# Kernel optimization log

Measured on AMD Instinct MI355X. Metric: run time of the kernel, lower is better.

The kernel has to match this reference:

```python
import jax, jax.numpy as jnp
import numpy as np


def _gauss_kernel(k, sigma):
    t = jnp.arange(k, dtype=jnp.float32) - (k - 1) / 2.0
    w = jnp.exp(-0.5 * (t / sigma) ** 2)
    return w / jnp.sum(w)


def setup_inputs() -> dict:
    key = jax.random.key(0)
    x = jax.random.normal(key, (8, 1, 16, 512, 512), dtype=jnp.float32)
    return {"x": x}


def _forward(x):
    b, c, n, h, w = x.shape
    imgs = x.reshape(b * n * c, 1, h, w)  # fuse batch/frame loop into one batched conv
    # Sobel-style vertical/horizontal 3x3 kernels (cross-correlation, as in torch F.conv2d)
    sobel = jnp.stack([
        jnp.array([[0., -1., 0.], [0., 0., 0.], [0., 1., 0.]], jnp.float32),
        jnp.array([[0., 0., 0.], [-1., 0., 1.], [0., 0., 0.]], jnp.float32),
    ])[:, None]  # (2,1,3,3)
    dn = jax.lax.conv_dimension_numbers(imgs.shape, sobel.shape, ('NCHW', 'OIHW', 'NCHW'))
    g = jax.lax.conv_general_dilated(imgs, sobel, (1, 1), [(1, 1), (1, 1)], dimension_numbers=dn)
    grad = jnp.sqrt(g[:, 0:1] ** 2 + g[:, 1:2] ** 2 + 1e-6)  # (b*n,1,h,w)
    # torchvision GaussianBlur(kernel_size=(7,13), sigma=(9,11)): ksize 7 along width,
    # 13 along height; sigma sampled U(9,11) at call time -> fixed to 10.0 for determinism.
    kx = _gauss_kernel(7, 10.0)
    ky = _gauss_kernel(13, 10.0)
    p = jnp.pad(grad, ((0, 0), (0, 0), (6, 6), (3, 3)), mode='reflect')  # torchvision reflect pad
    dnb = jax.lax.conv_dimension_numbers(p.shape, (1, 1, 1, 7), ('NCHW', 'OIHW', 'NCHW'))
    blur = jax.lax.conv_general_dilated(p, kx.reshape(1, 1, 1, 7), (1, 1), [(0, 0), (0, 0)], dimension_numbers=dnb)
    blur = jax.lax.conv_general_dilated(blur, ky.reshape(1, 1, 13, 1), (1, 1), [(0, 0), (0, 0)], dimension_numbers=dnb)
    # per-frame min/max normalization (torch.min/max over the whole single image)
    mn = jnp.min(blur, axis=(1, 2, 3), keepdims=True)
    mx = jnp.max(blur, axis=(1, 2, 3), keepdims=True)
    norm = (blur - mn) / (mx - mn)
    return norm.reshape(b, c, n, h, w)


def reference(x):
    norm = _forward(x)
    maskEdge = norm < 0.1
    maskNonEdge = norm >= 0.1
    return (maskEdge, maskNonEdge)
```

## Files before the change

### kernel.cpp

```cpp
#include <hip/hip_runtime.h>
#include <cmath>

static constexpr int IMH = 512;
static constexpr int IMW = 512;
static constexpr int IMG_PIX = IMH * IMW;

struct Weights {
    float kx[7];
    float ky[13];
};

__global__ void init_minmax_kernel(int* __restrict__ mm, int nimg) {
    int i = blockIdx.x * blockDim.x + threadIdx.x;
    if (i < nimg) {
        mm[2 * i]     = 0x7f7fffff;
        mm[2 * i + 1] = 0;
    }
}

template <int CTRL>
__device__ __forceinline__ float gm_dpp(float v) {
    return __int_as_float(__builtin_amdgcn_update_dpp(
        0, __float_as_int(v), CTRL, 0xF, 0xF, true));
}

__global__ __launch_bounds__(320, 6) void blur_kernel(
        const float* __restrict__ in, float* __restrict__ blur,
        int* __restrict__ mm, Weights wt) {
#pragma clang fp contract(off)
    const int band = blockIdx.x;
    const int img  = blockIdx.y;
    const int q    = threadIdx.x >> 6;
    const int lane = threadIdx.x & 63;
    const int cb   = band * 56 - 4;
    const int c    = cb + lane;
    int lc = c < 0 ? -c : (c > IMW - 1 ? 2 * (IMW - 1) - c : c);
    const bool cvalid = (lane >= 4) && (lane <= 59) && (c <= IMW - 1);
    const bool has_l  = (lc >= 1);
    const bool has_r  = (lc <= IMW - 2);

    const float* __restrict__ ip = in + (size_t)img * IMG_PIX;
    float* __restrict__ bp = blur + (size_t)img * IMG_PIX;

    const int gr0 = (q == 0) ? 0 : ((q == 1) ? 97 : ((q == 2) ? 200
                   : ((q == 3) ? 302 : 404)));
    const int tail_n = (q == 0) ? 5 : ((q == 1) ? 11 : ((q == 4) ? 4 : 10));
    const int tail_base = gr0 + 104;

    const float* xp = ip + (size_t)gr0 * IMW + lc;
    float x_m1 = (q == 0) ? 0.0f : xp[-IMW];
    float x_0  = xp[0];
    float x_p1 = xp[IMW];
    float x_p2 = xp[2 * (size_t)IMW];
    float x_p3 = xp[3 * (size_t)IMW];
    const float* xp_pref = xp + 4 * (size_t)IMW;
    float* op = bp + (size_t)(gr0 + 6) * IMW + c;

    float w[13];
    float tmn = 3.402823466e38f;
    float tmx = 0.0f;

#define GM_ROW(S, DO_OUT, DN, PREF)                                            \
    {                                                                          \
        float x_pf = (PREF);                                                   \
        float xl_ = gm_dpp<0x130>(x_0);                          \
        float xr_ = gm_dpp<0x138>(x_0);                          \
        float lf_ = has_l ? xl_ : 0.0f;                                        \
        float rt_ = has_r ? xr_ : 0.0f;                                        \
        float gv_ = (DN) - x_m1;                                               \
        float gh_ = rt_ - lf_;                                                 \
        float sg_ = gv_ * gv_ + gh_ * gh_;     \
        sg_ = sg_ + 1e-6f;                                                     \
        float g_ = sqrtf(sg_);                                                 \
        float gm1_ = gm_dpp<0x130>(g_);                                        \
        float gm2_ = gm_dpp<0x130>(gm1_);                                      \
        float gm3_ = gm_dpp<0x130>(gm2_);                                      \
        float gp1_ = gm_dpp<0x138>(g_);                                        \
        float gp2_ = gm_dpp<0x138>(gp1_);                                      \
        float gp3_ = gm_dpp<0x138>(gp2_);                                      \
        float ax_ = 0.0f;                                                      \
        ax_ += wt.kx[0] * gm3_;                                                \
        ax_ += wt.kx[1] * gm2_;                                                \
        ax_ += wt.kx[2] * gm1_;                                                \
        ax_ += wt.kx[3] * g_;                                                  \
        ax_ += wt.kx[4] * gp1_;                                                \
        ax_ += wt.kx[5] * gp2_;                                                \
        ax_ += wt.kx[6] * gp3_;                                                \
        w[(S) % 13] = ax_;                                                     \
        if (DO_OUT) {                                                          \
            float ay_ = 0.0f;                                                  \
            ay_ += wt.ky[0]  * w[((S) + 1)  % 13];                             \
            ay_ += wt.ky[1]  * w[((S) + 2)  % 13];                             \
            ay_ += wt.ky[2]  * w[((S) + 3)  % 13];                             \
            ay_ += wt.ky[3]  * w[((S) + 4)  % 13];                             \
            ay_ += wt.ky[4]  * w[((S) + 5)  % 13];                             \
            ay_ += wt.ky[5]  * w[((S) + 6)  % 13];                             \
            ay_ += wt.ky[6]  * w[((S) + 7)  % 13];                             \
            ay_ += wt.ky[7]  * w[((S) + 8)  % 13];                             \
            ay_ += wt.ky[8]  * w[((S) + 9)  % 13];                             \
            ay_ += wt.ky[9]  * w[((S) + 10) % 13];                             \
            ay_ += wt.ky[10] * w[((S) + 11) % 13];                             \
            ay_ += wt.ky[11] * w[((S) + 12) % 13];                             \
            ay_ += wt.ky[12] * w[((S) + 13) % 13];                             \
            if (cvalid) {                                                      \
                *op = ay_;                                                     \
                tmn = fminf(tmn, ay_);                                         \
                tmx = fmaxf(tmx, ay_);                                         \
            }                                                                  \
            op += IMW;                                                         \
        }                                                                      \
        x_m1 = x_0; x_0 = x_p1; x_p1 = x_p2; x_p2 = x_p3; x_p3 = x_pf;         \
        xp_pref += IMW;                                                        \
    }

    GM_ROW(0,  false, x_p1, xp_pref[0])
    GM_ROW(1,  false, x_p1, xp_pref[0])
    GM_ROW(2,  false, x_p1, xp_pref[0])
    GM_ROW(3,  false, x_p1, xp_pref[0])
    GM_ROW(4,  false, x_p1, xp_pref[0])
    GM_ROW(5,  false, x_p1, xp_pref[0])
    GM_ROW(6,  false, x_p1, xp_pref[0])
    GM_ROW(7,  false, x_p1, xp_pref[0])
    GM_ROW(8,  false, x_p1, xp_pref[0])
    GM_ROW(9,  false, x_p1, xp_pref[0])
    GM_ROW(10, false, x_p1, xp_pref[0])
    GM_ROW(11, false, x_p1, xp_pref[0])
    GM_ROW(12, true,  x_p1, xp_pref[0])

    if (q == 0) {
        #pragma unroll
        for (int orow = 0; orow < 6; ++orow) {
            float ay = 0.0f;
            #pragma unroll
            for (int j = 0; j < 13; ++j) {
                int t = orow + j - 6;
                t = t < 0 ? -t : t;
                ay += wt.ky[j] * w[t];
            }
            if (cvalid) {
                bp[(size_t)orow * IMW + c] = ay;
                tmn = fminf(tmn, ay);
                tmx = fmaxf(tmx, ay);
            }
        }
    }

    for (int giter = 0; giter < 7; ++giter) {
        GM_ROW(0,  true, x_p1, xp_pref[0])
        GM_ROW(1,  true, x_p1, xp_pref[0])
        GM_ROW(2,  true, x_p1, xp_pref[0])
        GM_ROW(3,  true, x_p1, xp_pref[0])
        GM_ROW(4,  true, x_p1, xp_pref[0])
        GM_ROW(5,  true, x_p1, xp_pref[0])
        GM_ROW(6,  true, x_p1, xp_pref[0])
        GM_ROW(7,  true, x_p1, xp_pref[0])
        GM_ROW(8,  true, x_p1, xp_pref[0])
        GM_ROW(9,  true, x_p1, xp_pref[0])
        GM_ROW(10, true, x_p1, xp_pref[0])
        GM_ROW(11, true, x_p1, xp_pref[0])
        GM_ROW(12, true, x_p1, xp_pref[0])
    }

#define GM_TAILROW(S)                                                          \
    if ((S) < tail_n) {                                                        \
        GM_ROW(S, true,                                                        \
               ((tail_base + (S)) == IMH - 1) ? 0.0f : x_p1,                   \
               ((tail_base + (S) + 4) <= IMH - 1) ? xp_pref[0] : 0.0f)         \
    }
    GM_TAILROW(0)
    GM_TAILROW(1)
    GM_TAILROW(2)
    GM_TAILROW(3)
    GM_TAILROW(4)
    GM_TAILROW(5)
    GM_TAILROW(6)
    GM_TAILROW(7)
    GM_TAILROW(8)
    GM_TAILROW(9)
    GM_TAILROW(10)
#undef GM_TAILROW
#undef GM_ROW

    if (q == 4) {
        #pragma unroll
        for (int oo = 0; oo < 6; ++oo) {
            int orow = 506 + oo;
            float ay = 0.0f;
            #pragma unroll
            for (int j = 0; j < 13; ++j) {
                int t = orow + j - 6;
                t = t > IMH - 1 ? 2 * (IMH - 1) - t : t;
                ay += wt.ky[j] * w[(t - 404) % 13];
            }
            if (cvalid) {
                bp[(size_t)orow * IMW + c] = ay;
                tmn = fminf(tmn, ay);
                tmx = fmaxf(tmx, ay);
            }
        }
    }

    #pragma unroll
    for (int off = 32; off > 0; off >>= 1) {
        tmn = fminf(tmn, __shfl_xor(tmn, off));
        tmx = fmaxf(tmx, __shfl_xor(tmx, off));
    }
    if (lane == 0) {
        atomicMin(&mm[2 * img], __float_as_int(tmn));
        atomicMax(&mm[2 * img + 1], __float_as_int(tmx));
    }
}

__global__ __launch_bounds__(256) void mask_kernel(
        const int* __restrict__ mm, int* __restrict__ edge,
        int* __restrict__ blurNe, long long n4) {
#pragma clang fp contract(off)
    const long long stride = (long long)gridDim.x * blockDim.x;
    for (long long i = (long long)blockIdx.x * blockDim.x + threadIdx.x;
         i < n4; i += stride) {
        int img = (int)(i >> 16);
        float mn = __int_as_float(mm[2 * img]);
        float mx = __int_as_float(mm[2 * img + 1]);
        float d = mx - mn;
        int4 vi = reinterpret_cast<const int4*>(blurNe)[i];
        float4 v = make_float4(__int_as_float(vi.x), __int_as_float(vi.y),
                               __int_as_float(vi.z), __int_as_float(vi.w));
        float n0 = (v.x - mn) / d;
        float n1 = (v.y - mn) / d;
        float n2 = (v.z - mn) / d;
        float n3 = (v.w - mn) / d;
        int4 e, ne;
        e.x = (n0 < 0.1f) ? 1 : 0;  ne.x = e.x ^ 1;
        e.y = (n1 < 0.1f) ? 1 : 0;  ne.y = e.y ^ 1;
        e.z = (n2 < 0.1f) ? 1 : 0;  ne.z = e.z ^ 1;
        e.w = (n3 < 0.1f) ? 1 : 0;  ne.w = e.w ^ 1;
        reinterpret_cast<int4*>(edge)[i] = e;
        reinterpret_cast<int4*>(blurNe)[i] = ne;
    }
}

extern "C" void kernel_launch(void* const* d_in, const int* in_sizes, int n_in,
                              void* d_out, int out_size, void* d_ws, size_t ws_size,
                              hipStream_t stream) {
    const float* x = (const float*)d_in[0];
    int* out = (int*)d_out;
    const long long N = (long long)in_sizes[0];
    const int nimg = (int)(N / IMG_PIX);
    float* blur = (float*)(out + N);
    int* mm = (int*)d_ws;

    Weights wt;
    {
        float tmp[13];
        float s = 0.0f;
        for (int i = 0; i < 7; ++i) {
            float t = (float)i - 3.0f;
            float u = t / 10.0f;
            tmp[i] = expf(-0.5f * (u * u));
            s += tmp[i];
        }
        for (int i = 0; i < 7; ++i) wt.kx[i] = tmp[i] / s;
        s = 0.0f;
        for (int i = 0; i < 13; ++i) {
            float t = (float)i - 6.0f;
            float u = t / 10.0f;
            tmp[i] = expf(-0.5f * (u * u));
            s += tmp[i];
        }
        for (int i = 0; i < 13; ++i) wt.ky[i] = tmp[i] / s;
    }

    init_minmax_kernel<<<1, 256, 0, stream>>>(mm, nimg);
    blur_kernel<<<dim3(10, nimg), 320, 0, stream>>>(x, blur, mm, wt);
    mask_kernel<<<4096, 256, 0, stream>>>(mm, out, (int*)blur, N / 4);
}
```

Before: 192.9 us.

## Deepen row prefetch to six rows and use nontemporal stores in mask kernel

The fused gradient/blur kernel now keeps two more input rows in flight (x_p4, x_p5), hiding more global load latency. Because the prefetch distance grew, the last quarter runs one fewer 13-row main iteration and handles the leftover rows in an extended tail. The mask kernel writes its outputs with nontemporal stores to avoid polluting cache with write-only data. The costs are extra registers and longer tail code with more predicated branches.

```diff
diff --git a/kernel.cpp b/kernel.cpp
--- a/kernel.cpp
+++ b/kernel.cpp
@@ -4,6 +4,8 @@
 static constexpr int IMH = 512;
 static constexpr int IMW = 512;
 static constexpr int IMG_PIX = IMH * IMW;
+
+typedef int nt_int4 __attribute__((ext_vector_type(4)));
 
 struct Weights {
     float kx[7];
@@ -44,8 +46,9 @@
 
     const int gr0 = (q == 0) ? 0 : ((q == 1) ? 97 : ((q == 2) ? 200
                    : ((q == 3) ? 302 : 404)));
-    const int tail_n = (q == 0) ? 5 : ((q == 1) ? 11 : ((q == 4) ? 4 : 10));
-    const int tail_base = gr0 + 104;
+    const int M         = (q == 4) ? 6 : 7;
+    const int tail_n    = (q == 0) ? 5 : ((q == 1) ? 11 : ((q == 4) ? 17 : 10));
+    const int tail_base = gr0 + 13 + 13 * M;
 
     const float* xp = ip + (size_t)gr0 * IMW + lc;
     float x_m1 = (q == 0) ? 0.0f : xp[-IMW];
@@ -53,7 +56,9 @@
     float x_p1 = xp[IMW];
     float x_p2 = xp[2 * (size_t)IMW];
     float x_p3 = xp[3 * (size_t)IMW];
-    const float* xp_pref = xp + 4 * (size_t)IMW;
+    float x_p4 = xp[4 * (size_t)IMW];
+    float x_p5 = xp[5 * (size_t)IMW];
+    const float* xp_pref = xp + 6 * (size_t)IMW;
     float* op = bp + (size_t)(gr0 + 6) * IMW + c;
 
     float w[13];
@@ -109,7 +114,8 @@
             }                                                                  \
             op += IMW;                                                         \
         }                                                                      \
-        x_m1 = x_0; x_0 = x_p1; x_p1 = x_p2; x_p2 = x_p3; x_p3 = x_pf;         \
+        x_m1 = x_0; x_0 = x_p1; x_p1 = x_p2; x_p2 = x_p3; x_p3 = x_p4;         \
+        x_p4 = x_p5; x_p5 = x_pf;                                              \
         xp_pref += IMW;                                                        \
     }
 
@@ -145,7 +151,7 @@
         }
     }
 
-    for (int giter = 0; giter < 7; ++giter) {
+    for (int giter = 0; giter < M; ++giter) {
         GM_ROW(0,  true, x_p1, xp_pref[0])
         GM_ROW(1,  true, x_p1, xp_pref[0])
         GM_ROW(2,  true, x_p1, xp_pref[0])
@@ -165,7 +171,7 @@
     if ((S) < tail_n) {                                                        \
         GM_ROW(S, true,                                                        \
                ((tail_base + (S)) == IMH - 1) ? 0.0f : x_p1,                   \
-               ((tail_base + (S) + 4) <= IMH - 1) ? xp_pref[0] : 0.0f)         \
+               ((tail_base + (S) + 6) <= IMH - 1) ? xp_pref[0] : 0.0f)         \
     }
     GM_TAILROW(0)
     GM_TAILROW(1)
@@ -178,6 +184,12 @@
     GM_TAILROW(8)
     GM_TAILROW(9)
     GM_TAILROW(10)
+    GM_TAILROW(11)
+    GM_TAILROW(12)
+    GM_TAILROW(13)
+    GM_TAILROW(14)
+    GM_TAILROW(15)
+    GM_TAILROW(16)
 #undef GM_TAILROW
 #undef GM_ROW
 
@@ -222,20 +234,18 @@
         float mn = __int_as_float(mm[2 * img]);
         float mx = __int_as_float(mm[2 * img + 1]);
         float d = mx - mn;
-        int4 vi = reinterpret_cast<const int4*>(blurNe)[i];
-        float4 v = make_float4(__int_as_float(vi.x), __int_as_float(vi.y),
-                               __int_as_float(vi.z), __int_as_float(vi.w));
-        float n0 = (v.x - mn) / d;
-        float n1 = (v.y - mn) / d;
-        float n2 = (v.z - mn) / d;
-        float n3 = (v.w - mn) / d;
-        int4 e, ne;
+        nt_int4 vi = *(reinterpret_cast<const nt_int4*>(blurNe) + i);
+        float n0 = (__int_as_float(vi.x) - mn) / d;
+        float n1 = (__int_as_float(vi.y) - mn) / d;
+        float n2 = (__int_as_float(vi.z) - mn) / d;
+        float n3 = (__int_as_float(vi.w) - mn) / d;
+        nt_int4 e, ne;
         e.x = (n0 < 0.1f) ? 1 : 0;  ne.x = e.x ^ 1;
         e.y = (n1 < 0.1f) ? 1 : 0;  ne.y = e.y ^ 1;
         e.z = (n2 < 0.1f) ? 1 : 0;  ne.z = e.z ^ 1;
         e.w = (n3 < 0.1f) ? 1 : 0;  ne.w = e.w ^ 1;
-        reinterpret_cast<int4*>(edge)[i] = e;
-        reinterpret_cast<int4*>(blurNe)[i] = ne;
+        __builtin_nontemporal_store(e, reinterpret_cast<nt_int4*>(edge) + i);
+        __builtin_nontemporal_store(ne, reinterpret_cast<nt_int4*>(blurNe) + i);
     }
 }
 
```

Result: faster. 163.5 us (median of 2 runs) (-15.3%).
